# Optimization experiments

Measured on AMD Instinct MI355X. Metric: run time of the kernel, lower is better.

Reference implementation:

```python
import jax, jax.numpy as jnp
import numpy as np

B_GRAPHS = 256      # graphs per batch
NPG = 256           # nodes per graph
EXTENT = 32.0       # coordinate extent
K1 = 5              # kernel size per dim
KK = K1 * K1        # 25 weight matrices (dim=2)


def _cartesian(pos, row, col, ev):
    # pseudo-coords: relative cartesian, globally rescaled into [0,1]
    d = pos[col] - pos[row]                                   # [E,2]
    m = jnp.max(jnp.where(ev[:, None] > 0, jnp.abs(d), 0.0))
    return d / (2.0 * m + 1e-12) + 0.5


def _spline_conv(x, row, col, pseudo, ev, W, root, bias, n):
    # degree-1 open B-spline basis, 4 nonzero corners per edge (dim=2)
    v = pseudo * (K1 - 1)
    i0 = jnp.clip(jnp.floor(v), 0, K1 - 2).astype(jnp.int32)  # [E,2]
    f = v - i0
    xin = x[col]                                              # [E,Fin] gather
    acc = jnp.zeros((n * KK, x.shape[1]), x.dtype)
    for sx in (0, 1):
        for sy in (0, 1):
            idx = (i0[:, 0] + sx) * K1 + (i0[:, 1] + sy)      # flat kernel id
            wx = f[:, 0] if sx else 1.0 - f[:, 0]
            wy = f[:, 1] if sy else 1.0 - f[:, 1]
            b = wx * wy * ev
            acc = acc.at[row * KK + idx].add(b[:, None] * xin)
    acc = acc.reshape(n, KK, x.shape[1])                      # [n,25,Fin]
    deg = jax.ops.segment_sum(ev, row, num_segments=n)
    out = jnp.einsum('nki,kio->no', acc, W) / jnp.maximum(deg, 1.0)[:, None]
    return out + x @ root + bias


def _grid_pool(x, pos, row, col, ev, nv, size):
    g = int(EXTENT // size)
    c = jnp.clip(jnp.floor(pos / size).astype(jnp.int32), 0, g - 1)
    cluster = (jnp.arange(x.shape[0], dtype=jnp.int32) * 0)  # placeholder
    cell = c[:, 0] * g + c[:, 1]
    nb = x.shape[0] // 1  # nodes
    # batch id of each node = node's graph; recover from fixed layout
    # (cluster id = graph * g*g + cell)
    per_graph = nb // B_GRAPHS
    gb = jnp.arange(nb, dtype=jnp.int32) // per_graph
    cluster = gb * (g * g) + cell
    Nc = B_GRAPHS * g * g
    seg = jnp.where(nv > 0, cluster, Nc)                      # invalid -> dummy
    xm = jax.ops.segment_max(jnp.where(nv[:, None] > 0, x, -jnp.inf), seg,
                             num_segments=Nc + 1)[:Nc]
    cnt = jax.ops.segment_sum(nv, seg, num_segments=Nc + 1)[:Nc]
    nv2 = (cnt > 0).astype(x.dtype)
    x2 = jnp.where(nv2[:, None] > 0, xm, 0.0)
    pos2 = jax.ops.segment_sum(pos * nv[:, None], seg, num_segments=Nc + 1)[:Nc]
    pos2 = pos2 / jnp.maximum(cnt, 1.0)[:, None]
    batch2 = jnp.arange(Nc, dtype=jnp.int32) // (g * g)
    # remap + coalesce edges (drop self-loops and duplicates, fixed shapes)
    r2 = cluster[row]
    c2 = cluster[col]
    ev2 = (ev > 0) & (r2 != c2)
    key = jnp.where(ev2, r2 * Nc + c2, Nc * Nc)
    order = jnp.argsort(key)
    skey = key[order]
    dup = jnp.concatenate([jnp.zeros((1,), bool), skey[1:] == skey[:-1]])
    ev3 = ((skey < Nc * Nc) & ~dup).astype(x.dtype)
    return x2, pos2, r2[order], c2[order], ev3, batch2, nv2


def _forward(x, position, edge_index, batch, W1, root1, b1, W2, root2, b2,
             W3, root3, b3, fc_w, fc_b):
    row, col = edge_index[0], edge_index[1]
    E, N = row.shape[0], x.shape[0]
    ev = jnp.ones((E,), x.dtype)
    nv = jnp.ones((N,), x.dtype)
    ps = _cartesian(position, row, col, ev)
    h = jax.nn.elu(_spline_conv(x, row, col, ps, ev, W1, root1, b1, N))
    h, pos, row, col, ev, batch2, nv = _grid_pool(h, position, row, col, ev, nv, 4.0)
    ps = _cartesian(pos, row, col, ev)
    h = jax.nn.elu(_spline_conv(h, row, col, ps, ev, W2, root2, b2, h.shape[0]))
    h, pos, row, col, ev, batch2, nv = _grid_pool(h, pos, row, col, ev, nv, 8.0)
    ps = _cartesian(pos, row, col, ev)
    h = jax.nn.elu(_spline_conv(h, row, col, ps, ev, W3, root3, b3, h.shape[0]))
    # scatter_mean over graphs (only non-empty clusters count)
    gsum = jax.ops.segment_sum(h * nv[:, None], batch2, num_segments=B_GRAPHS)
    gcnt = jax.ops.segment_sum(nv, batch2, num_segments=B_GRAPHS)
    gfeat = gsum / jnp.maximum(gcnt, 1.0)[:, None]
    # dropout is identity in eval mode
    logits = gfeat @ fc_w + fc_b
    return jax.nn.log_softmax(logits, axis=1)


def setup_inputs() -> dict:
    DEG = 16
    N = B_GRAPHS * NPG
    E = N * DEG
    key = jax.random.key(0)
    ks = jax.random.split(key, 14)
    x = jax.random.uniform(ks[0], (N, 1), jnp.float32)
    position = jax.random.uniform(ks[1], (N, 2), jnp.float32) * EXTENT
    src = jax.random.randint(ks[2], (E,), 0, N, dtype=jnp.int32)
    tgt = (src // NPG) * NPG + jax.random.randint(ks[3], (E,), 0, NPG, dtype=jnp.int32)
    edge_index = jnp.stack([tgt, src])  # row = target, col = source
    batch = jnp.arange(N, dtype=jnp.int32) // NPG
    s = 0.1
    W1 = jax.random.normal(ks[4], (KK, 1, 32), jnp.float32) * s
    root1 = jax.random.normal(ks[5], (1, 32), jnp.float32) * s
    b1 = jnp.zeros((32,), jnp.float32)
    W2 = jax.random.normal(ks[6], (KK, 32, 64), jnp.float32) * s
    root2 = jax.random.normal(ks[7], (32, 64), jnp.float32) * s
    b2 = jnp.zeros((64,), jnp.float32)
    W3 = jax.random.normal(ks[8], (KK, 64, 128), jnp.float32) * s
    root3 = jax.random.normal(ks[9], (64, 128), jnp.float32) * s
    b3 = jnp.zeros((128,), jnp.float32)
    fc_w = jax.random.normal(ks[10], (128, 10), jnp.float32) * s
    fc_b = jnp.zeros((10,), jnp.float32)
    return dict(x=x, position=position, edge_index=edge_index, batch=batch,
                W1=W1, root1=root1, b1=b1, W2=W2, root2=root2, b2=b2,
                W3=W3, root3=root3, b3=b3, fc_w=fc_w, fc_b=fc_b)


def reference(x, position, edge_index, batch, W1, root1, b1, W2, root2, b2,
              W3, root3, b3, fc_w, fc_b):
    return _forward(x, position, edge_index, batch, W1, root1, b1,
                    W2, root2, b2, W3, root3, b3, fc_w, fc_b)
```

## Files before the change

### kernel.cpp

```cpp
#include <hip/hip_runtime.h>
#include <math.h>

constexpr int NN  = 65536;
constexpr int EE  = 1048576;
constexpr int NG  = 256;
constexpr int NC1 = 16384;
constexpr int NC2 = 4096;
constexpr int EPB = EE / 256;

constexpr size_t O_SCAL  = 0;
constexpr size_t O_GTOT  = 256;
constexpr size_t O_CNT2  = O_GTOT + 1024;
constexpr size_t O_PS2   = O_CNT2 + (size_t)NC2*4;
constexpr size_t Z_END   = O_PS2  + (size_t)NC2*8;
constexpr size_t O_XM2   = Z_END;
constexpr size_t O_GOFF  = O_XM2  + (size_t)NC2*64*4;
constexpr size_t O_BB    = O_GOFF + 1280;
constexpr size_t O_BE    = O_BB   + (size_t)256*256*4;
constexpr size_t O_XP1   = O_BE   + (size_t)EE*2;
constexpr size_t O_POS1  = O_XP1  + (size_t)NC1*32*4;
constexpr size_t O_NV1   = O_POS1 + (size_t)NC1*8;
constexpr size_t O_ADJ2  = O_NV1  + (size_t)NC1*4;
constexpr size_t O_OFF2S = O_ADJ2 + (size_t)NG*4096;
constexpr size_t O_DEG2I = O_OFF2S+ (size_t)NC1*4;
constexpr size_t O_CL2   = O_DEG2I+ (size_t)NC1*4;
constexpr size_t O_XP2   = O_CL2  + (size_t)NC1*4;
constexpr size_t O_POS2  = O_XP2  + (size_t)NC2*64*4;
constexpr size_t O_NV2   = O_POS2 + (size_t)NC2*8;
constexpr size_t O_ADJ3  = O_NV2  + (size_t)NC2*4;
constexpr size_t O_OFF3S = O_ADJ3 + (size_t)NG*256;
constexpr size_t O_DEG3I = O_OFF3S+ (size_t)NC2*4;
constexpr size_t O_H3    = O_DEG3I+ (size_t)NC2*4;
constexpr size_t O_W2Q   = O_H3   + (size_t)NC2*128*4;
constexpr size_t O_W3Q   = O_W2Q  + 102400;
constexpr size_t O_RT2   = O_W3Q  + 409600;
constexpr size_t O_RT3   = O_RT2  + 4096;

typedef __fp16   pk16x2 __attribute__((ext_vector_type(2)));
typedef _Float16 f16x8  __attribute__((ext_vector_type(8)));
typedef float    f32x4  __attribute__((ext_vector_type(4)));

__device__ __forceinline__ float eluf(float x){ return x > 0.f ? x : expm1f(x); }

__device__ __forceinline__ void atomic_max_pos(float* a, float v){
    atomicMax((unsigned int*)a, __float_as_uint(v));
}
__device__ __forceinline__ void atomic_max_f32(float* a, float v){
    unsigned int b = __float_as_uint(v);
    if (b & 0x80000000u) atomicMin((unsigned int*)a, b);
    else                 atomicMax((int*)a, (int)b);
}

__device__ __forceinline__ unsigned int pack2(float a, float b){
    pk16x2 h = __builtin_amdgcn_cvt_pkrtz(a, b);
    return __builtin_bit_cast(unsigned int, h);
}
__device__ __forceinline__ f32x4 mfma16(uint4 a, uint4 b, f32x4 c){
    return __builtin_amdgcn_mfma_f32_16x16x32_f16(
        __builtin_bit_cast(f16x8, a), __builtin_bit_cast(f16x8, b), c, 0, 0, 0);
}

struct Crn { int ix, iy; float fx, fy; };
__device__ __forceinline__ Crn mk_corners(float dx, float dy, float m){
    float inv = 1.0f / (2.0f*m + 1e-12f);
    float vx = (dx*inv + 0.5f) * 4.0f;
    float vy = (dy*inv + 0.5f) * 4.0f;
    Crn c;
    c.ix = min(max((int)floorf(vx), 0), 3);
    c.iy = min(max((int)floorf(vy), 0), 3);
    c.fx = vx - (float)c.ix;
    c.fy = vy - (float)c.iy;
    return c;
}

#define BLOCK_MAX_AND_ATOMIC(val, dst)                                   \
    {   __shared__ float _s[256];                                        \
        _s[threadIdx.x] = (val); __syncthreads();                        \
        for (int _w = 128; _w > 0; _w >>= 1){                            \
            if (threadIdx.x < _w)                                        \
                _s[threadIdx.x] = fmaxf(_s[threadIdx.x], _s[threadIdx.x+_w]); \
            __syncthreads();                                             \
        }                                                                \
        if (threadIdx.x == 0) atomic_max_pos((dst), _s[0]); }

__global__ __launch_bounds__(256) void k_pass1(
        const int* __restrict__ ei, const float* __restrict__ pos,
        float* m1, int* gtot, int* bb,
        const float* __restrict__ W2, const float* __restrict__ W3,
        const float* __restrict__ root2, const float* __restrict__ root3,
        unsigned int* __restrict__ w2q, unsigned int* __restrict__ w3q,
        unsigned int* __restrict__ rt2q, unsigned int* __restrict__ rt3q){
    __shared__ int h[256];
    if (blockIdx.x >= 256){
        int idx = (blockIdx.x - 256)*256 + threadIdx.x;
        if (idx < 25600){
            int tt = idx/6400, r = idx%6400, i = r/256, r2 = r%256;
            int l = r2>>2, j = r2&3;
            int o = tt*16 + (l&15);
            int Kb = i*32 + (l>>4)*8 + 2*j;
            w2q[idx] = pack2(W2[Kb*64 + o], W2[(Kb+1)*64 + o]);
        } else if (idx < 128000){
            int d = idx - 25600;
            int tt = d/12800, r = d%12800, kc = r/256, r2 = r%256;
            int l = r2>>2, j = r2&3;
            int o = tt*16 + (l&15);
            int Kb = kc*32 + (l>>4)*8 + 2*j;
            w3q[d] = pack2(W3[Kb*128 + o], W3[(Kb+1)*128 + o]);
        } else if (idx < 129024){
            int d = idx - 128000;
            int tt = d/256, r2 = d%256, l = r2>>2, j = r2&3;
            int o = tt*16 + (l&15);
            int k = (l>>4)*8 + 2*j;
            rt2q[d] = pack2(root2[k*64 + o], root2[(k+1)*64 + o]);
        } else if (idx < 133120){
            int d = idx - 129024;
            int tt = d/512, kc = (d/256)&1, r2 = d%256, l = r2>>2, j = r2&3;
            int o = tt*16 + (l&15);
            int k = kc*32 + (l>>4)*8 + 2*j;
            rt3q[d] = pack2(root3[k*128 + o], root3[(k+1)*128 + o]);
        }
        return;
    }
    h[threadIdx.x] = 0; __syncthreads();
    int base = blockIdx.x * EPB;
    float loc = 0.f;
    for (int i = threadIdx.x; i < EPB; i += 256){
        int e = base + i;
        int r = ei[e], c = ei[EE + e];
        float dx = pos[2*c]   - pos[2*r];
        float dy = pos[2*c+1] - pos[2*r+1];
        loc = fmaxf(loc, fmaxf(fabsf(dx), fabsf(dy)));
        atomicAdd(&h[r >> 8], 1);
    }
    __syncthreads();
    bb[blockIdx.x*256 + threadIdx.x] = atomicAdd(&gtot[threadIdx.x], h[threadIdx.x]);
    BLOCK_MAX_AND_ATOMIC(loc, m1);
}

__global__ void k_gscan(const int* __restrict__ gtot, int* goff){
    __shared__ int s[256];
    int t = threadIdx.x;
    int v0 = gtot[t];
    s[t] = v0; __syncthreads();
    for (int d = 1; d < 256; d <<= 1){
        int u = (t >= d) ? s[t-d] : 0;
        __syncthreads();
        s[t] += u;
        __syncthreads();
    }
    goff[t] = s[t] - v0;
    if (t == 255) goff[256] = s[t];
}

__global__ __launch_bounds__(256) void k_pass2(const int* __restrict__ ei,
                                               const int* __restrict__ goff,
                                               const int* __restrict__ bb,
                                               unsigned short* __restrict__ be){
    __shared__ int cur[256];
    cur[threadIdx.x] = 0; __syncthreads();
    int base = blockIdx.x * EPB;
    for (int i = threadIdx.x; i < EPB; i += 256){
        int e = base + i;
        int r = ei[e], c = ei[EE + e];
        int g = r >> 8;
        int l = atomicAdd(&cur[g], 1);
        be[goff[g] + bb[blockIdx.x*256 + g] + l] =
            (unsigned short)((r & 255) | ((c & 255) << 8));
    }
}

__global__ __launch_bounds__(1024) void k_graph1(
        const unsigned short* __restrict__ be, const int* __restrict__ goff,
        const float* __restrict__ pos, const float* __restrict__ x,
        const float* __restrict__ m1p, const float* __restrict__ W1,
        const float* __restrict__ root1, const float* __restrict__ b1,
        float* __restrict__ xp1, float* __restrict__ pos1g, float* __restrict__ nv1,
        unsigned char* __restrict__ adj2b, int* __restrict__ off2s,
        int* __restrict__ deg2i, float* m2p){
    __shared__ float acc[256*25];
    __shared__ float posx[256], posy[256], xL[256];
    __shared__ int   cl1L[256], degL[256];
    __shared__ float sW[800];
    __shared__ unsigned int bitL[128];
    __shared__ float xmL[64*32];
    __shared__ int   cntL[64];
    __shared__ float psx[64], psy[64];
    __shared__ float p1x[64], p1y[64];
    __shared__ int   rpre[64];
    __shared__ float mred[64];

    int t = threadIdx.x, g = blockIdx.x;
    if (t < 800) sW[t] = W1[t];
    for (int i = t; i < 6400; i += 1024) acc[i] = 0.f;
    if (t < 256){
        float px = pos[2*(g*256 + t)], py = pos[2*(g*256 + t) + 1];
        posx[t] = px; posy[t] = py;
        xL[t]   = x[g*256 + t];
        degL[t] = 0;
        int cx = min(max((int)floorf(px*0.25f), 0), 7);
        int cy = min(max((int)floorf(py*0.25f), 0), 7);
        cl1L[t] = cx*8 + cy;
    }
    if (t < 128) bitL[t] = 0u;
    if (t < 64){ cntL[t] = 0; psx[t] = 0.f; psy[t] = 0.f; }
    for (int i = t; i < 2048; i += 1024) xmL[i] = -INFINITY;
    __syncthreads();

    float mm = *m1p;
    int e1 = goff[g+1];
    for (int p = goff[g] + t; p < e1; p += 1024){
        unsigned int b = be[p];
        int rl = b & 255, cl = (b >> 8) & 255;
        float dx = posx[cl] - posx[rl], dy = posy[cl] - posy[rl];
        Crn cr = mk_corners(dx, dy, mm);
        float xin = xL[cl];
        int ab = rl*25 + cr.ix*5 + cr.iy;
        atomicAdd(&acc[ab],   (1.f-cr.fx)*(1.f-cr.fy)*xin);
        atomicAdd(&acc[ab+1], (1.f-cr.fx)*cr.fy*xin);
        atomicAdd(&acc[ab+5], cr.fx*(1.f-cr.fy)*xin);
        atomicAdd(&acc[ab+6], cr.fx*cr.fy*xin);
        atomicAdd(&degL[rl], 1);
        int r2 = cl1L[rl], c2 = cl1L[cl];
        if (r2 != c2){
            int bit = r2*64 + c2;
            atomicOr(&bitL[bit >> 5], 1u << (bit & 31));
        }
    }
    __syncthreads();

    {
        int n = t >> 2, q = t & 3;
        float accR[25];
        #pragma unroll
        for (int k = 0; k < 25; k++) accR[k] = acc[n*25 + k];
        float inv = 1.f / fmaxf((float)degL[n], 1.f);
        float xr  = xL[n];
        int   cl  = cl1L[n];
        if (q == 0){
            atomicAdd(&cntL[cl], 1);
            atomicAdd(&psx[cl], posx[n]);
            atomicAdd(&psy[cl], posy[n]);
        }
        #pragma unroll
        for (int oo = 0; oo < 8; oo++){
            int o = q*8 + oo;
            float s = 0.f;
            #pragma unroll
            for (int k = 0; k < 25; k++) s += accR[k]*sW[k*32 + o];
            float out = eluf(s*inv + xr*root1[o] + b1[o]);
            atomic_max_f32(&xmL[cl*32 + o], out);
        }
    }
    __syncthreads();

    if (t < 64){
        float cnt = (float)cntL[t];
        float inv = 1.f / fmaxf(cnt, 1.f);
        p1x[t] = psx[t]*inv; p1y[t] = psy[t]*inv;
        pos1g[2*(g*64 + t)]     = p1x[t];
        pos1g[2*(g*64 + t) + 1] = p1y[t];
        nv1[g*64 + t] = (cnt > 0.f) ? 1.f : 0.f;
    }
    __syncthreads();
    for (int i = t; i < 2048; i += 1024){
        int c = i >> 5;
        xp1[g*2048 + i] = (cntL[c] > 0) ? xmL[i] : 0.f;
    }

    if (t < 64) rpre[t] = __popc(bitL[2*t]) + __popc(bitL[2*t+1]);
    __syncthreads();
    for (int d = 1; d < 64; d <<= 1){
        int v = 0;
        if (t < 64 && t >= d) v = rpre[t-d];
        __syncthreads();
        if (t < 64) rpre[t] += v;
        __syncthreads();
    }
    float m2loc = 0.f;
    if (t < 64){
        unsigned int w0 = bitL[2*t], w1 = bitL[2*t+1];
        int dg = __popc(w0) + __popc(w1);
        int baseo = rpre[t] - dg;
        off2s[g*64 + t] = g*4096 + baseo;
        deg2i[g*64 + t] = dg;
        int j = g*4096 + baseo;
        float rx = p1x[t], ry = p1y[t];
        while (w0){
            int b = __ffs(w0) - 1; w0 &= w0 - 1;
            adj2b[j++] = (unsigned char)b;
            m2loc = fmaxf(m2loc, fmaxf(fabsf(p1x[b]-rx), fabsf(p1y[b]-ry)));
        }
        while (w1){
            int b = __ffs(w1) - 1; w1 &= w1 - 1;
            int c = 32 + b;
            adj2b[j++] = (unsigned char)c;
            m2loc = fmaxf(m2loc, fmaxf(fabsf(p1x[c]-rx), fabsf(p1y[c]-ry)));
        }
        mred[t] = m2loc;
    }
    __syncthreads();
    if (t == 0){
        float v = mred[0];
        for (int i = 1; i < 64; i++) v = fmaxf(v, mred[i]);
        atomic_max_pos(m2p, v);
    }
}

__global__ __launch_bounds__(512) void k_conv2(
        const int* __restrict__ off2s, const int* __restrict__ deg2i,
        const unsigned char* __restrict__ adj2b, const float* __restrict__ pos1g,
        const float* __restrict__ m2p, const float* __restrict__ xp1,
        const unsigned int* __restrict__ wq2, const unsigned int* __restrict__ rt2q,
        const float* __restrict__ b2, const float* __restrict__ nv1,
        int* __restrict__ cl2, float* cnt2, float* ps2, float* xm2){
    __shared__ unsigned int amu[16*404];
    __shared__ float xpL[64*32];
    __shared__ unsigned int xq[16*20];
    __shared__ float pc[8*256];
    __shared__ float p1x[64], p1y[64];
    int t = threadIdx.x;
    int g = blockIdx.x >> 2, sub = blockIdx.x & 3;
    for (int i = t; i < 2048; i += 512) xpL[i] = xp1[g*2048 + i];
    if (t < 64){ p1x[t] = pos1g[2*(g*64+t)]; p1y[t] = pos1g[2*(g*64+t)+1]; }
    __syncthreads();
    if (t < 256){
        int m = t >> 4, jj = t & 15;
        int c = sub*16 + m;
        xq[m*20 + jj] = pack2(xpL[c*32 + 2*jj], xpL[c*32 + 2*jj + 1]);
    }
    int grp = t >> 5, lane = t & 31;
    {
        int rl = sub*16 + grp;
        int r  = g*64 + rl;
        int s0 = off2s[r], nd = deg2i[r];
        float rx = p1x[rl], ry = p1y[rl];
        float invm = 1.0f / (2.0f*(*m2p) + 1e-12f);
        float acc[25];
        #pragma unroll
        for (int k = 0; k < 25; k++) acc[k] = 0.f;
        for (int base = 0; base < nd; base += 32){
            int e = base + lane;
            int myc = 0;
            float wxl[5], wyl[5];
            #pragma unroll
            for (int k = 0; k < 5; k++){ wxl[k] = 0.f; wyl[k] = 0.f; }
            if (e < nd){
                myc = adj2b[s0 + e];
                float vx = ((p1x[myc]-rx)*invm + 0.5f)*4.0f;
                float vy = ((p1y[myc]-ry)*invm + 0.5f)*4.0f;
                #pragma unroll
                for (int k = 0; k < 5; k++){
                    wxl[k] = fmaxf(0.f, 1.f - fabsf(vx - (float)k));
                    wyl[k] = fmaxf(0.f, 1.f - fabsf(vy - (float)k));
                }
            }
            int cnt = min(32, nd - base);
            for (int j = 0; j < cnt; ++j){
                int c = __shfl(myc, j, 32);
                float xin = xpL[c*32 + lane];
                float xv[5], yv[5];
                #pragma unroll
                for (int k = 0; k < 5; k++){
                    xv[k] = __shfl(wxl[k], j, 32) * xin;
                    yv[k] = __shfl(wyl[k], j, 32);
                }
                #pragma unroll
                for (int kx = 0; kx < 5; kx++)
                    #pragma unroll
                    for (int ky = 0; ky < 5; ky++)
                        acc[kx*5+ky] = fmaf(xv[kx], yv[ky], acc[kx*5+ky]);
            }
        }
        float invd = 1.f / fmaxf((float)nd, 1.f);
        unsigned int* dst = &amu[grp*404];
        #pragma unroll
        for (int k = 0; k < 25; k++){
            float a = acc[k]*invd;
            float o2 = __shfl_xor(a, 1, 64);
            if (!(lane & 1)) dst[k*16 + (lane >> 1)] = pack2(a, o2);
        }
    }
    __syncthreads();
    {
        int w = t >> 6, l = t & 63;
        int tt = w & 3, kh = w >> 2;
        int m = l & 15, kb = l >> 4;
        f32x4 cacc = {0.f, 0.f, 0.f, 0.f};
        int ks0 = kh ? 12 : 0, ks1 = kh ? 25 : 12;
        for (int i = ks0; i < ks1; ++i){
            uint4 au = *(const uint4*)&amu[m*404 + i*16 + kb*4];
            uint4 bu = *(const uint4*)&wq2[((tt*25 + i)*64 + l)*4];
            cacc = mfma16(au, bu, cacc);
        }
        if (kh == 0){
            uint4 au = *(const uint4*)&xq[m*20 + kb*4];
            uint4 bu = *(const uint4*)&rt2q[(tt*64 + l)*4];
            cacc = mfma16(au, bu, cacc);
        }
        *(f32x4*)&pc[w*256 + l*4] = cacc;
    }
    __syncthreads();
    {
        int tt = t >> 7, q = t & 127;
        int l = q & 63, rh = q >> 6;
        #pragma unroll
        for (int u = 0; u < 2; ++u){
            int r_ = rh*2 + u;
            int m = (l >> 4)*4 + r_;
            int o = tt*16 + (l & 15);
            float val = pc[tt*256 + l*4 + r_] + pc[(tt+4)*256 + l*4 + r_];
            val = eluf(val + b2[o]);
            int rl = sub*16 + m;
            int rr = g*64 + rl;
            float px = p1x[rl], py = p1y[rl];
            int cx = min(max((int)floorf(px*0.125f), 0), 3);
            int cy = min(max((int)floorf(py*0.125f), 0), 3);
            int cl = g*16 + cx*4 + cy;
            float nv = nv1[rr];
            if (o == 0){
                cl2[rr] = cl;
                if (nv > 0.f){
                    atomicAdd(&cnt2[cl], 1.f);
                    atomicAdd(&ps2[2*cl],   px);
                    atomicAdd(&ps2[2*cl+1], py);
                }
            }
            if (nv > 0.f) atomic_max_f32(&xm2[cl*64 + o], val);
        }
    }
}

__global__ __launch_bounds__(256) void k_lvl3(
        const int* __restrict__ off2s, const int* __restrict__ deg2i,
        const unsigned char* __restrict__ adj2b, const int* __restrict__ cl2,
        const float* __restrict__ cnt2, const float* __restrict__ ps2,
        const float* __restrict__ xm2,
        float* __restrict__ xp2, float* __restrict__ pos2g, float* __restrict__ nv2,
        unsigned char* __restrict__ adj3b, int* __restrict__ off3s,
        int* __restrict__ deg3i, float* m3p){
    __shared__ int cl2L[64];
    __shared__ unsigned int bit3[8];
    __shared__ float p2x[16], p2y[16];
    __shared__ int rpre[16];
    int t = threadIdx.x, g = blockIdx.x;
    if (t < 64) cl2L[t] = cl2[g*64 + t] & 15;
    if (t < 8)  bit3[t] = 0u;
    if (t < 16){
        float cnt = cnt2[g*16 + t];
        float inv = 1.f / fmaxf(cnt, 1.f);
        p2x[t] = ps2[2*(g*16+t)]*inv;
        p2y[t] = ps2[2*(g*16+t)+1]*inv;
        pos2g[2*(g*16+t)]   = p2x[t];
        pos2g[2*(g*16+t)+1] = p2y[t];
        nv2[g*16 + t] = (cnt > 0.f) ? 1.f : 0.f;
    }
    for (int i = t; i < 1024; i += 256){
        int c = i >> 6;
        xp2[g*1024 + i] = (cnt2[g*16 + c] > 0.f) ? xm2[g*1024 + i] : 0.f;
    }
    __syncthreads();
    if (t < 64){
        int s0 = off2s[g*64 + t], n = deg2i[g*64 + t];
        int r3 = cl2L[t];
        for (int j = 0; j < n; ++j){
            int c3 = cl2L[adj2b[s0 + j]];
            if (r3 != c3){
                int bit = r3*16 + c3;
                atomicOr(&bit3[bit >> 5], 1u << (bit & 31));
            }
        }
    }
    __syncthreads();
    if (t < 16)
        rpre[t] = __popc((bit3[t >> 1] >> ((t & 1)*16)) & 0xFFFFu);
    __syncthreads();
    for (int d = 1; d < 16; d <<= 1){
        int v = 0;
        if (t < 16 && t >= d) v = rpre[t-d];
        __syncthreads();
        if (t < 16) rpre[t] += v;
        __syncthreads();
    }
    float m3loc = 0.f;
    if (t < 16){
        unsigned int w = (bit3[t >> 1] >> ((t & 1)*16)) & 0xFFFFu;
        int dg = __popc(w);
        int baseo = rpre[t] - dg;
        off3s[g*16 + t] = g*256 + baseo;
        deg3i[g*16 + t] = dg;
        int j = g*256 + baseo;
        float rx = p2x[t], ry = p2y[t];
        while (w){
            int b = __ffs(w) - 1; w &= w - 1;
            adj3b[j++] = (unsigned char)b;
            m3loc = fmaxf(m3loc, fmaxf(fabsf(p2x[b]-rx), fabsf(p2y[b]-ry)));
        }
    }
    BLOCK_MAX_AND_ATOMIC(m3loc, m3p);
}

__global__ __launch_bounds__(512) void k_conv3(
        const int* __restrict__ off3s, const int* __restrict__ deg3i,
        const unsigned char* __restrict__ adj3b, const float* __restrict__ pos2g,
        const float* __restrict__ m3p, const float* __restrict__ xp2,
        const unsigned int* __restrict__ wq3, const unsigned int* __restrict__ rt3q,
        const float* __restrict__ b3, float* __restrict__ h3){
    __shared__ unsigned int amu[16*804];
    __shared__ float xpL[16*64];
    __shared__ unsigned int xq[16*36];
    __shared__ float p2x[16], p2y[16];
    int t = threadIdx.x, g = blockIdx.x;
    for (int i = t; i < 1024; i += 512) xpL[i] = xp2[g*1024 + i];
    if (t < 16){ p2x[t] = pos2g[2*(g*16+t)]; p2y[t] = pos2g[2*(g*16+t)+1]; }
    __syncthreads();
    {
        int m = t >> 5, jj = t & 31;
        xq[m*36 + jj] = pack2(xpL[m*64 + 2*jj], xpL[m*64 + 2*jj + 1]);
    }
    int grp = t >> 6, lane = t & 63;
    float invm = 1.0f / (2.0f*(*m3p) + 1e-12f);
    for (int cc = 0; cc < 2; ++cc){
        int rl = grp + cc*8;
        int r  = g*16 + rl;
        int s0 = off3s[r], nd = deg3i[r];
        float rx = p2x[rl], ry = p2y[rl];
        float acc[25];
        #pragma unroll
        for (int k = 0; k < 25; k++) acc[k] = 0.f;
        for (int base = 0; base < nd; base += 64){
            int e = base + lane;
            int myc = 0;
            float wxl[5], wyl[5];
            #pragma unroll
            for (int k = 0; k < 5; k++){ wxl[k] = 0.f; wyl[k] = 0.f; }
            if (e < nd){
                myc = adj3b[s0 + e];
                float vx = ((p2x[myc]-rx)*invm + 0.5f)*4.0f;
                float vy = ((p2y[myc]-ry)*invm + 0.5f)*4.0f;
                #pragma unroll
                for (int k = 0; k < 5; k++){
                    wxl[k] = fmaxf(0.f, 1.f - fabsf(vx - (float)k));
                    wyl[k] = fmaxf(0.f, 1.f - fabsf(vy - (float)k));
                }
            }
            int cnt = min(64, nd - base);
            for (int j = 0; j < cnt; ++j){
                int c = __shfl(myc, j, 64);
                float xin = xpL[c*64 + lane];
                float xv[5], yv[5];
                #pragma unroll
                for (int k = 0; k < 5; k++){
                    xv[k] = __shfl(wxl[k], j, 64) * xin;
                    yv[k] = __shfl(wyl[k], j, 64);
                }
                #pragma unroll
                for (int kx = 0; kx < 5; kx++)
                    #pragma unroll
                    for (int ky = 0; ky < 5; ky++)
                        acc[kx*5+ky] = fmaf(xv[kx], yv[ky], acc[kx*5+ky]);
            }
        }
        float invd = 1.f / fmaxf((float)nd, 1.f);
        unsigned int* dst = &amu[rl*804];
        #pragma unroll
        for (int k = 0; k < 25; k++){
            float a = acc[k]*invd;
            float o2 = __shfl_xor(a, 1, 64);
            if (!(lane & 1)) dst[k*32 + (lane >> 1)] = pack2(a, o2);
        }
    }
    __syncthreads();
    {
        int w = t >> 6, l = t & 63;
        int m = l & 15, kb = l >> 4;
        f32x4 cacc = {0.f, 0.f, 0.f, 0.f};
        for (int kc = 0; kc < 50; ++kc){
            uint4 au = *(const uint4*)&amu[m*804 + kc*16 + kb*4];
            uint4 bu = *(const uint4*)&wq3[((w*50 + kc)*64 + l)*4];
            cacc = mfma16(au, bu, cacc);
        }
        #pragma unroll
        for (int kc = 0; kc < 2; ++kc){
            uint4 au = *(const uint4*)&xq[m*36 + kc*16 + kb*4];
            uint4 bu = *(const uint4*)&rt3q[((w*2 + kc)*64 + l)*4];
            cacc = mfma16(au, bu, cacc);
        }
        int o = w*16 + (l & 15);
        float bb3 = b3[o];
        #pragma unroll
        for (int r_ = 0; r_ < 4; ++r_){
            int m2_ = (l >> 4)*4 + r_;
            h3[(g*16 + m2_)*128 + o] = eluf(cacc[r_] + bb3);
        }
    }
}

__global__ void k_readout(const float* __restrict__ h3, const float* __restrict__ nv2,
                          const float* __restrict__ fcw, const float* __restrict__ fcb,
                          float* out){
    int g = blockIdx.x, t = threadIdx.x;
    __shared__ float gf[128];
    __shared__ float lg[10];
    __shared__ float lse;
    float s = 0.f, cnt = 0.f;
    for (int j = 0; j < 16; j++){
        int c = g*16 + j;
        float nv = nv2[c];
        s += h3[c*128 + t] * nv;
        cnt += nv;
    }
    gf[t] = s / fmaxf(cnt, 1.f);
    __syncthreads();
    if (t < 10){
        float l = fcb[t];
        for (int f = 0; f < 128; f++) l += gf[f]*fcw[f*10 + t];
        lg[t] = l;
    }
    __syncthreads();
    if (t == 0){
        float mx = -INFINITY;
        for (int o = 0; o < 10; o++) mx = fmaxf(mx, lg[o]);
        float ss = 0.f;
        for (int o = 0; o < 10; o++) ss += expf(lg[o] - mx);
        lse = mx + logf(ss);
    }
    __syncthreads();
    if (t < 10) out[g*10 + t] = lg[t] - lse;
}

extern "C" void kernel_launch(void* const* d_in, const int* in_sizes, int n_in,
                              void* d_out, int out_size, void* d_ws, size_t ws_size,
                              hipStream_t stream){
    const float* x     = (const float*)d_in[0];
    const float* posi  = (const float*)d_in[1];
    const int*   ei    = (const int*)  d_in[2];
    const float* W1    = (const float*)d_in[4];
    const float* root1 = (const float*)d_in[5];
    const float* b1    = (const float*)d_in[6];
    const float* W2    = (const float*)d_in[7];
    const float* root2 = (const float*)d_in[8];
    const float* b2    = (const float*)d_in[9];
    const float* W3    = (const float*)d_in[10];
    const float* root3 = (const float*)d_in[11];
    const float* b3    = (const float*)d_in[12];
    const float* fcw   = (const float*)d_in[13];
    const float* fcb   = (const float*)d_in[14];
    float* out = (float*)d_out;

    char* ws = (char*)d_ws;
    float*          m1    = (float*)(ws + O_SCAL);
    float*          m2    = m1 + 1;
    float*          m3    = m1 + 2;
    int*            gtot  = (int*)  (ws + O_GTOT);
    float*          cnt2  = (float*)(ws + O_CNT2);
    float*          ps2   = (float*)(ws + O_PS2);
    float*          xm2   = (float*)(ws + O_XM2);
    int*            goff  = (int*)  (ws + O_GOFF);
    int*            bb    = (int*)  (ws + O_BB);
    unsigned short* be    = (unsigned short*)(ws + O_BE);
    float*          xp1   = (float*)(ws + O_XP1);
    float*          pos1g = (float*)(ws + O_POS1);
    float*          nv1   = (float*)(ws + O_NV1);
    unsigned char*  adj2b = (unsigned char*)(ws + O_ADJ2);
    int*            off2s = (int*)  (ws + O_OFF2S);
    int*            deg2i = (int*)  (ws + O_DEG2I);
    int*            cl2   = (int*)  (ws + O_CL2);
    float*          xp2   = (float*)(ws + O_XP2);
    float*          pos2g = (float*)(ws + O_POS2);
    float*          nv2   = (float*)(ws + O_NV2);
    unsigned char*  adj3b = (unsigned char*)(ws + O_ADJ3);
    int*            off3s = (int*)  (ws + O_OFF3S);
    int*            deg3i = (int*)  (ws + O_DEG3I);
    float*          h3    = (float*)(ws + O_H3);
    unsigned int*   w2q   = (unsigned int*)(ws + O_W2Q);
    unsigned int*   w3q   = (unsigned int*)(ws + O_W3Q);
    unsigned int*   rt2q  = (unsigned int*)(ws + O_RT2);
    unsigned int*   rt3q  = (unsigned int*)(ws + O_RT3);

    hipMemsetAsync(ws, 0, Z_END, stream);
    hipMemsetAsync(xm2, 0xFF, (size_t)NC2*64*4, stream);

    k_pass1<<<256 + 520, 256, 0, stream>>>(ei, posi, m1, gtot, bb,
                                           W2, W3, root2, root3, w2q, w3q, rt2q, rt3q);
    k_gscan<<<1, 256, 0, stream>>>(gtot, goff);
    k_pass2<<<256, 256, 0, stream>>>(ei, goff, bb, be);

    k_graph1<<<NG, 1024, 0, stream>>>(be, goff, posi, x, m1, W1, root1, b1,
                                      xp1, pos1g, nv1, adj2b, off2s, deg2i, m2);

    k_conv2<<<NC1/16, 512, 0, stream>>>(off2s, deg2i, adj2b, pos1g, m2, xp1,
                                        w2q, rt2q, b2, nv1, cl2, cnt2, ps2, xm2);

    k_lvl3<<<NG, 256, 0, stream>>>(off2s, deg2i, adj2b, cl2, cnt2, ps2, xm2,
                                   xp2, pos2g, nv2, adj3b, off3s, deg3i, m3);

    k_conv3<<<NG, 512, 0, stream>>>(off3s, deg3i, adj3b, pos2g, m3, xp2,
                                    w3q, rt3q, b3, h3);

    k_readout<<<256, 128, 0, stream>>>(h3, nv2, fcw, fcb, out);
}
```

Before: 274.6 us.

## Stage basis weights in LDS, simplify conv2 MFMA epilogue, split conv3 across blocks

In conv2 and conv3 the per-edge B-spline weights and neighbour ids are now packed as fp16 into shared memory, replacing per-edge warp shuffles. conv2 also caps each row at 64 neighbours in two chunks, drops the K-split MFMA with its partial-sum reduction buffer, and runs 4 waves doing the full K loop with a direct epilogue. conv3 is launched with twice as many blocks, each handling 8 rows, which doubles parallelism but leaves half of each MFMA tile as zero padding. The fp16 weights add rounding error, and the fixed two-chunk loop assumes degree never exceeds 64.

```diff
diff --git a/kernel.cpp b/kernel.cpp
--- a/kernel.cpp
+++ b/kernel.cpp
@@ -37,6 +37,7 @@
 constexpr size_t O_RT3   = O_RT2  + 4096;
 
 typedef __fp16   pk16x2 __attribute__((ext_vector_type(2)));
+typedef _Float16 h16x2  __attribute__((ext_vector_type(2)));
 typedef _Float16 f16x8  __attribute__((ext_vector_type(8)));
 typedef float    f32x4  __attribute__((ext_vector_type(4)));
 
@@ -54,6 +55,10 @@
 __device__ __forceinline__ unsigned int pack2(float a, float b){
     pk16x2 h = __builtin_amdgcn_cvt_pkrtz(a, b);
     return __builtin_bit_cast(unsigned int, h);
+}
+__device__ __forceinline__ float2 unpk(unsigned int u){
+    h16x2 h = __builtin_bit_cast(h16x2, u);
+    return make_float2((float)h[0], (float)h[1]);
 }
 __device__ __forceinline__ f32x4 mfma16(uint4 a, uint4 b, f32x4 c){
     return __builtin_amdgcn_mfma_f32_16x16x32_f16(
@@ -316,7 +321,7 @@
     __shared__ unsigned int amu[16*404];
     __shared__ float xpL[64*32];
     __shared__ unsigned int xq[16*20];
-    __shared__ float pc[8*256];
+    __shared__ unsigned int wbuf[6][512];
     __shared__ float p1x[64], p1y[64];
     int t = threadIdx.x;
     int g = blockIdx.x >> 2, sub = blockIdx.x & 3;
@@ -329,48 +334,59 @@
         xq[m*20 + jj] = pack2(xpL[c*32 + 2*jj], xpL[c*32 + 2*jj + 1]);
     }
     int grp = t >> 5, lane = t & 31;
-    {
-        int rl = sub*16 + grp;
-        int r  = g*64 + rl;
-        int s0 = off2s[r], nd = deg2i[r];
-        float rx = p1x[rl], ry = p1y[rl];
-        float invm = 1.0f / (2.0f*(*m2p) + 1e-12f);
-        float acc[25];
-        #pragma unroll
-        for (int k = 0; k < 25; k++) acc[k] = 0.f;
-        for (int base = 0; base < nd; base += 32){
+    int rl = sub*16 + grp;
+    int r  = g*64 + rl;
+    int s0 = off2s[r], nd = deg2i[r];
+    float rx = p1x[rl], ry = p1y[rl];
+    float invm = 1.0f / (2.0f*(*m2p) + 1e-12f);
+    float acc[25];
+    #pragma unroll
+    for (int k = 0; k < 25; k++) acc[k] = 0.f;
+    #pragma unroll
+    for (int chunk = 0; chunk < 2; ++chunk){
+        int base = chunk*32;
+        {
             int e = base + lane;
-            int myc = 0;
-            float wxl[5], wyl[5];
-            #pragma unroll
-            for (int k = 0; k < 5; k++){ wxl[k] = 0.f; wyl[k] = 0.f; }
+            unsigned int u0=0,u1=0,u2=0,u3=0,u4=0,uc=0;
             if (e < nd){
-                myc = adj2b[s0 + e];
-                float vx = ((p1x[myc]-rx)*invm + 0.5f)*4.0f;
-                float vy = ((p1y[myc]-ry)*invm + 0.5f)*4.0f;
+                int cc = adj2b[s0 + e];
+                float vx = ((p1x[cc]-rx)*invm + 0.5f)*4.0f;
+                float vy = ((p1y[cc]-ry)*invm + 0.5f)*4.0f;
+                float wx[5], wy[5];
                 #pragma unroll
                 for (int k = 0; k < 5; k++){
-                    wxl[k] = fmaxf(0.f, 1.f - fabsf(vx - (float)k));
-                    wyl[k] = fmaxf(0.f, 1.f - fabsf(vy - (float)k));
+                    wx[k] = fmaxf(0.f, 1.f - fabsf(vx - (float)k));
+                    wy[k] = fmaxf(0.f, 1.f - fabsf(vy - (float)k));
                 }
+                u0 = pack2(wx[0], wx[1]); u1 = pack2(wx[2], wx[3]);
+                u2 = pack2(wx[4], wy[0]); u3 = pack2(wy[1], wy[2]);
+                u4 = pack2(wy[3], wy[4]); uc = (unsigned int)cc;
             }
-            int cnt = min(32, nd - base);
-            for (int j = 0; j < cnt; ++j){
-                int c = __shfl(myc, j, 32);
-                float xin = xpL[c*32 + lane];
-                float xv[5], yv[5];
+            wbuf[0][t]=u0; wbuf[1][t]=u1; wbuf[2][t]=u2;
+            wbuf[3][t]=u3; wbuf[4][t]=u4; wbuf[5][t]=uc;
+        }
+        __syncthreads();
+        int cnt = min(32, nd - base);
+        for (int j = 0; j < cnt; ++j){
+            int idx = grp*32 + j;
+            float2 a0 = unpk(wbuf[0][idx]);
+            float2 a1 = unpk(wbuf[1][idx]);
+            float2 a2 = unpk(wbuf[2][idx]);
+            float2 a3 = unpk(wbuf[3][idx]);
+            float2 a4 = unpk(wbuf[4][idx]);
+            int c = (int)wbuf[5][idx];
+            float xin = xpL[c*32 + lane];
+            float xv[5] = {a0.x*xin, a0.y*xin, a1.x*xin, a1.y*xin, a2.x*xin};
+            float yv[5] = {a2.y, a3.x, a3.y, a4.x, a4.y};
+            #pragma unroll
+            for (int kx = 0; kx < 5; kx++)
                 #pragma unroll
-                for (int k = 0; k < 5; k++){
-                    xv[k] = __shfl(wxl[k], j, 32) * xin;
-                    yv[k] = __shfl(wyl[k], j, 32);
-                }
-                #pragma unroll
-                for (int kx = 0; kx < 5; kx++)
-                    #pragma unroll
-                    for (int ky = 0; ky < 5; ky++)
-                        acc[kx*5+ky] = fmaf(xv[kx], yv[ky], acc[kx*5+ky]);
-            }
-        }
+                for (int ky = 0; ky < 5; ky++)
+                    acc[kx*5+ky] = fmaf(xv[kx], yv[ky], acc[kx*5+ky]);
+        }
+        __syncthreads();
+    }
+    {
         float invd = 1.f / fmaxf((float)nd, 1.f);
         unsigned int* dst = &amu[grp*404];
         #pragma unroll
@@ -381,38 +397,29 @@
         }
     }
     __syncthreads();
-    {
+    if (t < 256){
         int w = t >> 6, l = t & 63;
-        int tt = w & 3, kh = w >> 2;
         int m = l & 15, kb = l >> 4;
         f32x4 cacc = {0.f, 0.f, 0.f, 0.f};
-        int ks0 = kh ? 12 : 0, ks1 = kh ? 25 : 12;
-        for (int i = ks0; i < ks1; ++i){
+        for (int i = 0; i < 25; ++i){
             uint4 au = *(const uint4*)&amu[m*404 + i*16 + kb*4];
-            uint4 bu = *(const uint4*)&wq2[((tt*25 + i)*64 + l)*4];
+            uint4 bu = *(const uint4*)&wq2[((w*25 + i)*64 + l)*4];
             cacc = mfma16(au, bu, cacc);
         }
-        if (kh == 0){
+        {
             uint4 au = *(const uint4*)&xq[m*20 + kb*4];
-            uint4 bu = *(const uint4*)&rt2q[(tt*64 + l)*4];
+            uint4 bu = *(const uint4*)&rt2q[(w*64 + l)*4];
             cacc = mfma16(au, bu, cacc);
         }
-        *(f32x4*)&pc[w*256 + l*4] = cacc;
-    }
-    __syncthreads();
-    {
-        int tt = t >> 7, q = t & 127;
-        int l = q & 63, rh = q >> 6;
+        int o = w*16 + (l & 15);
+        float bb = b2[o];
         #pragma unroll
-        for (int u = 0; u < 2; ++u){
-            int r_ = rh*2 + u;
-            int m = (l >> 4)*4 + r_;
-            int o = tt*16 + (l & 15);
-            float val = pc[tt*256 + l*4 + r_] + pc[(tt+4)*256 + l*4 + r_];
-            val = eluf(val + b2[o]);
-            int rl = sub*16 + m;
-            int rr = g*64 + rl;
-            float px = p1x[rl], py = p1y[rl];
+        for (int r_ = 0; r_ < 4; ++r_){
+            int mrow = (l >> 4)*4 + r_;
+            float val = eluf(cacc[r_] + bb);
+            int rl2 = sub*16 + mrow;
+            int rr = g*64 + rl2;
+            float px = p1x[rl2], py = p1y[rl2];
             int cx = min(max((int)floorf(px*0.125f), 0), 3);
             int cy = min(max((int)floorf(py*0.125f), 0), 3);
             int cl = g*16 + cx*4 + cy;
@@ -505,63 +512,72 @@
         const float* __restrict__ m3p, const float* __restrict__ xp2,
         const unsigned int* __restrict__ wq3, const unsigned int* __restrict__ rt3q,
         const float* __restrict__ b3, float* __restrict__ h3){
-    __shared__ unsigned int amu[16*804];
+    __shared__ unsigned int amu[8*804];
     __shared__ float xpL[16*64];
-    __shared__ unsigned int xq[16*36];
+    __shared__ unsigned int xq[8*36];
+    __shared__ unsigned int wbuf[6][128];
     __shared__ float p2x[16], p2y[16];
-    int t = threadIdx.x, g = blockIdx.x;
+    int t = threadIdx.x;
+    int g = blockIdx.x >> 1, sub = blockIdx.x & 1;
     for (int i = t; i < 1024; i += 512) xpL[i] = xp2[g*1024 + i];
     if (t < 16){ p2x[t] = pos2g[2*(g*16+t)]; p2y[t] = pos2g[2*(g*16+t)+1]; }
     __syncthreads();
+    if (t < 256){
+        int m = t >> 5, jj = t & 31;
+        int c = sub*8 + m;
+        xq[m*36 + jj] = pack2(xpL[c*64 + 2*jj], xpL[c*64 + 2*jj + 1]);
+    }
+    int grp = t >> 6, lane = t & 63;
+    int rl = sub*8 + grp;
+    int r  = g*16 + rl;
+    int s0 = off3s[r], nd = deg3i[r];
+    float rx = p2x[rl], ry = p2y[rl];
+    float invm = 1.0f / (2.0f*(*m3p) + 1e-12f);
+    if (lane < 16){
+        int e = lane;
+        unsigned int u0=0,u1=0,u2=0,u3=0,u4=0,uc=0;
+        if (e < nd){
+            int cc = adj3b[s0 + e];
+            float vx = ((p2x[cc]-rx)*invm + 0.5f)*4.0f;
+            float vy = ((p2y[cc]-ry)*invm + 0.5f)*4.0f;
+            float wx[5], wy[5];
+            #pragma unroll
+            for (int k = 0; k < 5; k++){
+                wx[k] = fmaxf(0.f, 1.f - fabsf(vx - (float)k));
+                wy[k] = fmaxf(0.f, 1.f - fabsf(vy - (float)k));
+            }
+            u0 = pack2(wx[0], wx[1]); u1 = pack2(wx[2], wx[3]);
+            u2 = pack2(wx[4], wy[0]); u3 = pack2(wy[1], wy[2]);
+            u4 = pack2(wy[3], wy[4]); uc = (unsigned int)cc;
+        }
+        int idx = grp*16 + e;
+        wbuf[0][idx]=u0; wbuf[1][idx]=u1; wbuf[2][idx]=u2;
+        wbuf[3][idx]=u3; wbuf[4][idx]=u4; wbuf[5][idx]=uc;
+    }
+    __syncthreads();
+    float acc[25];
+    #pragma unroll
+    for (int k = 0; k < 25; k++) acc[k] = 0.f;
+    for (int j = 0; j < nd; ++j){
+        int idx = grp*16 + j;
+        float2 a0 = unpk(wbuf[0][idx]);
+        float2 a1 = unpk(wbuf[1][idx]);
+        float2 a2 = unpk(wbuf[2][idx]);
+        float2 a3 = unpk(wbuf[3][idx]);
+        float2 a4 = unpk(wbuf[4][idx]);
+        int c = (int)wbuf[5][idx];
+        float xin = xpL[c*64 + lane];
+        float xv[5] = {a0.x*xin, a0.y*xin, a1.x*xin, a1.y*xin, a2.x*xin};
+        float yv[5] = {a2.y, a3.x, a3.y, a4.x, a4.y};
+        #pragma unroll
+        for (int kx = 0; kx < 5; kx++)
+            #pragma unroll
+            for (int ky = 0; ky < 5; ky++)
+                acc[kx*5+ky] = fmaf(xv[kx], yv[ky], acc[kx*5+ky]);
+    }
     {
-        int m = t >> 5, jj = t & 31;
-        xq[m*36 + jj] = pack2(xpL[m*64 + 2*jj], xpL[m*64 + 2*jj + 1]);
-    }
-    int grp = t >> 6, lane = t & 63;
-    float invm = 1.0f / (2.0f*(*m3p) + 1e-12f);
-    for (int cc = 0; cc < 2; ++cc){
-        int rl = grp + cc*8;
-        int r  = g*16 + rl;
-        int s0 = off3s[r], nd = deg3i[r];
-        float rx = p2x[rl], ry = p2y[rl];
-        float acc[25];
-        #pragma unroll
-        for (int k = 0; k < 25; k++) acc[k] = 0.f;
-        for (int base = 0; base < nd; base += 64){
-            int e = base + lane;
-            int myc = 0;
-            float wxl[5], wyl[5];
-            #pragma unroll
-            for (int k = 0; k < 5; k++){ wxl[k] = 0.f; wyl[k] = 0.f; }
-            if (e < nd){
-                myc = adj3b[s0 + e];
-                float vx = ((p2x[myc]-rx)*invm + 0.5f)*4.0f;
-                float vy = ((p2y[myc]-ry)*invm + 0.5f)*4.0f;
-                #pragma unroll
-                for (int k = 0; k < 5; k++){
-                    wxl[k] = fmaxf(0.f, 1.f - fabsf(vx - (float)k));
-                    wyl[k] = fmaxf(0.f, 1.f - fabsf(vy - (float)k));
-                }
-            }
-            int cnt = min(64, nd - base);
-            for (int j = 0; j < cnt; ++j){
-                int c = __shfl(myc, j, 64);
-                float xin = xpL[c*64 + lane];
-                float xv[5], yv[5];
-                #pragma unroll
-                for (int k = 0; k < 5; k++){
-                    xv[k] = __shfl(wxl[k], j, 64) * xin;
-                    yv[k] = __shfl(wyl[k], j, 64);
-                }
-                #pragma unroll
-                for (int kx = 0; kx < 5; kx++)
-                    #pragma unroll
-                    for (int ky = 0; ky < 5; ky++)
-                        acc[kx*5+ky] = fmaf(xv[kx], yv[ky], acc[kx*5+ky]);
-            }
-        }
         float invd = 1.f / fmaxf((float)nd, 1.f);
-        unsigned int* dst = &amu[rl*804];
+        unsigned int* dst = &amu[grp*804];
         #pragma unroll
         for (int k = 0; k < 25; k++){
             float a = acc[k]*invd;
@@ -575,22 +591,25 @@
         int m = l & 15, kb = l >> 4;
         f32x4 cacc = {0.f, 0.f, 0.f, 0.f};
         for (int kc = 0; kc < 50; ++kc){
-            uint4 au = *(const uint4*)&amu[m*804 + kc*16 + kb*4];
+            uint4 au = {0u,0u,0u,0u};
+            if (m < 8) au = *(const uint4*)&amu[m*804 + kc*16 + kb*4];
             uint4 bu = *(const uint4*)&wq3[((w*50 + kc)*64 + l)*4];
             cacc = mfma16(au, bu, cacc);
         }
         #pragma unroll
         for (int kc = 0; kc < 2; ++kc){
-            uint4 au = *(const uint4*)&xq[m*36 + kc*16 + kb*4];
+            uint4 au = {0u,0u,0u,0u};
+            if (m < 8) au = *(const uint4*)&xq[m*36 + kc*16 + kb*4];
             uint4 bu = *(const uint4*)&rt3q[((w*2 + kc)*64 + l)*4];
             cacc = mfma16(au, bu, cacc);
         }
         int o = w*16 + (l & 15);
-        float bb3 = b3[o];
+        float bb = b3[o];
         #pragma unroll
         for (int r_ = 0; r_ < 4; ++r_){
-            int m2_ = (l >> 4)*4 + r_;
-            h3[(g*16 + m2_)*128 + o] = eluf(cacc[r_] + bb3);
+            int mrow = (l >> 4)*4 + r_;
+            if (mrow < 8)
+                h3[(g*16 + sub*8 + mrow)*128 + o] = eluf(cacc[r_] + bb);
         }
     }
 }
@@ -694,8 +713,8 @@
     k_lvl3<<<NG, 256, 0, stream>>>(off2s, deg2i, adj2b, cl2, cnt2, ps2, xm2,
                                    xp2, pos2g, nv2, adj3b, off3s, deg3i, m3);
 
-    k_conv3<<<NG, 512, 0, stream>>>(off3s, deg3i, adj3b, pos2g, m3, xp2,
-                                    w3q, rt3q, b3, h3);
+    k_conv3<<<NG*2, 512, 0, stream>>>(off3s, deg3i, adj3b, pos2g, m3, xp2,
+                                      w3q, rt3q, b3, h3);
 
     k_readout<<<256, 128, 0, stream>>>(h3, nv2, fcw, fcb, out);
 }
```

New measurement: 246.7 us. 10.2% less time.
